# Kernel tuning notes

Hardware: AMD Instinct MI355X
Metric: run time of the kernel (lower is better)

Reference implementation:

```python
import jax, jax.numpy as jnp
import numpy as np

N = 8192
IN_F = 256
OUT_F = 128
ALPHA = 0.2  # LeakyReLU negative slope
NEG = -1e12


def setup_inputs() -> dict:
    key = jax.random.key(0)
    k1, k2, k3, k4, k5, k6 = jax.random.split(key, 6)
    inp = jax.random.normal(k1, (N, IN_F), dtype=jnp.float32)
    adj = jax.random.randint(k2, (N, N), 0, 2, dtype=jnp.int32)
    # xavier_uniform with gain=1.414
    def xavier(k, shape, gain=1.414):
        fan_in, fan_out = shape[0], shape[1]
        bound = gain * np.sqrt(6.0 / (fan_in + fan_out))
        return jax.random.uniform(k, shape, jnp.float32, -bound, bound)
    W = xavier(k3, (IN_F, OUT_F))
    a = xavier(k4, (2 * OUT_F, 1))
    W_2 = xavier(k5, (IN_F, OUT_F))
    a_2 = xavier(k6, (2 * OUT_F, 1))
    return {"inp": inp, "adj": adj, "W": W, "a": a, "W_2": W_2, "a_2": a_2}


def _gat_head(h, a_vec, mask):
    # Equivalent to e[i,j] = leakyrelu(a^T [h_i ; h_j]) without N^2*2F concat:
    # split a into source/destination halves.
    a_src = a_vec[:OUT_F, 0]   # [F]
    a_dst = a_vec[OUT_F:, 0]   # [F]
    e = (h @ a_src)[:, None] + (h @ a_dst)[None, :]        # [N, N]
    e = jnp.where(e > 0, e, ALPHA * e)                      # LeakyReLU
    e = jnp.where(mask, e, NEG)
    att = jax.nn.softmax(e, axis=1)                         # [N, N]
    # dropout omitted (eval mode, training=False)
    return att @ h                                          # [N, F]


def reference(inp, adj, W, a, W_2, a_2):
    h = inp @ W      # [N, F]
    h_2 = inp @ W_2  # [N, F]
    mask = adj > 0   # adj is nonneg ints so adj*adj>0 is the same mask
    h_prime = _gat_head(h, a, mask)
    h_prime_2 = _gat_head(h_2, a_2, mask)
    h_total = h_prime + 0.5 * h_prime_2
    return jax.nn.elu(h_total)  # concat=True
```

## Files before the change

### kernel.cpp

```cpp
#include <hip/hip_runtime.h>
#include <hip/hip_fp16.h>

#define NN 8192
#define INF 256
#define OUTF 128
#define LOG2E 1.44269504088896340736f

typedef float f32x4 __attribute__((ext_vector_type(4)));
typedef float f32x16 __attribute__((ext_vector_type(16)));
typedef __fp16 h16x8 __attribute__((ext_vector_type(8)));
typedef __fp16 h16x4 __attribute__((ext_vector_type(4)));
typedef __fp16 h16x2 __attribute__((ext_vector_type(2)));
typedef int i32x4 __attribute__((ext_vector_type(4)));

__device__ __forceinline__ void gload_lds16(const void* g, void* l) {
  __builtin_amdgcn_global_load_lds(
      (const __attribute__((address_space(1))) unsigned int*)g,
      (__attribute__((address_space(3))) unsigned int*)l, 16, 0, 0);
}

__device__ __forceinline__ unsigned encf(float f) {
  int b = __float_as_int(f);
  return b >= 0 ? ((unsigned)b | 0x80000000u) : ~(unsigned)b;
}
__device__ __forceinline__ float decf(unsigned u) {
  int b = (u & 0x80000000u) ? (int)(u & 0x7FFFFFFFu) : ~(int)u;
  return __int_as_float(b);
}

__global__ __launch_bounds__(256) void kb_pack(const int* __restrict__ adj,
                                               unsigned short* __restrict__ adjb) {
  int gid = blockIdx.x * 256 + threadIdx.x;
#pragma unroll
  for (int it = 0; it < 8; ++it) {
    size_t c = (size_t)it * 524288 + gid;
    const int* p = adj + c * 16;
    i32x4 v0 = *(const i32x4*)(p);
    i32x4 v1 = *(const i32x4*)(p + 4);
    i32x4 v2 = *(const i32x4*)(p + 8);
    i32x4 v3 = *(const i32x4*)(p + 12);
    unsigned int b = 0;
#pragma unroll
    for (int k = 0; k < 4; ++k) {
      b |= (v0[k] != 0 ? 1u : 0u) << k;
      b |= (v1[k] != 0 ? 1u : 0u) << (4 + k);
      b |= (v2[k] != 0 ? 1u : 0u) << (8 + k);
      b |= (v3[k] != 0 ? 1u : 0u) << (12 + k);
    }
    adjb[c] = (unsigned short)b;
  }
}

__global__ __launch_bounds__(256) void k0_wt(const float* __restrict__ W1,
                                             const float* __restrict__ W2,
                                             __fp16* __restrict__ WT,
                                             unsigned* __restrict__ GMu) {
  if (blockIdx.x == 0 && threadIdx.x < 2) GMu[threadIdx.x] = 0u;
  int m = blockIdx.x * 256 + threadIdx.x;
  int h = m >> 12;
  int r = m & 4095;
  int c = r >> 5;
  int kb = (r >> 1) & 15;
  int hh = r & 1;
  const float* W = h ? W2 : W1;
  float v[8];
#pragma unroll
  for (int s = 0; s < 8; ++s) {
    int koff = 4 * hh + (s & 3) + 8 * (s >> 2);
    v[s] = W[(kb * 16 + koff) * OUTF + c];
  }
  union { h16x2 h2[4]; i32x4 q; } u;
  u.h2[0] = __builtin_amdgcn_cvt_pkrtz(v[0], v[1]);
  u.h2[1] = __builtin_amdgcn_cvt_pkrtz(v[2], v[3]);
  u.h2[2] = __builtin_amdgcn_cvt_pkrtz(v[4], v[5]);
  u.h2[3] = __builtin_amdgcn_cvt_pkrtz(v[6], v[7]);
  *(i32x4*)(WT + (size_t)h * 32768 + c * 256 + kb * 16 + hh * 8) = u.q;
}

__global__ __launch_bounds__(128) void k1_h(
    const float* __restrict__ inp, const __fp16* __restrict__ WT,
    const float* __restrict__ a1, const float* __restrict__ a2,
    __fp16* __restrict__ hT2, float* __restrict__ S, float* __restrict__ D,
    unsigned* __restrict__ GMu) {
  __shared__ __align__(16) float hl[2][32][136];
  int tid = threadIdx.x;
  int w = tid >> 6;
  int l = tid & 63;
  int lr = l & 31, g = l >> 5;
  int i0 = blockIdx.x * 32;
  const __fp16* WTh = WT + (size_t)w * 32768;
  f32x16 acc[4];
#pragma unroll
  for (int nf = 0; nf < 4; ++nf)
#pragma unroll
    for (int e = 0; e < 16; ++e) acc[nf][e] = 0.0f;
  const float* ip = inp + (size_t)(i0 + lr) * INF;
#pragma unroll
  for (int kb = 0; kb < 16; ++kb) {
    f32x4 q0 = *(const f32x4*)(ip + kb * 16 + 4 * g);
    f32x4 q1 = *(const f32x4*)(ip + kb * 16 + 8 + 4 * g);
    union { h16x2 h2[4]; h16x8 h8; } ua;
    ua.h2[0] = __builtin_amdgcn_cvt_pkrtz(q0[0], q0[1]);
    ua.h2[1] = __builtin_amdgcn_cvt_pkrtz(q0[2], q0[3]);
    ua.h2[2] = __builtin_amdgcn_cvt_pkrtz(q1[0], q1[1]);
    ua.h2[3] = __builtin_amdgcn_cvt_pkrtz(q1[2], q1[3]);
#pragma unroll
    for (int nf = 0; nf < 4; ++nf) {
      h16x8 b = *(const h16x8*)(WTh + (nf * 32 + lr) * 256 + kb * 16 + g * 8);
      acc[nf] = __builtin_amdgcn_mfma_f32_32x32x16_f16(ua.h8, b, acc[nf], 0, 0, 0);
    }
  }
#pragma unroll
  for (int nf = 0; nf < 4; ++nf)
#pragma unroll
    for (int r = 0; r < 16; ++r) {
      int row = (r & 3) + 8 * (r >> 2) + 4 * g;
      hl[w][row][nf * 32 + lr] = acc[nf][r];
    }
  __syncthreads();
  const float* av = w ? a2 : a1;
  float s = 0.f, d = 0.f;
#pragma unroll
  for (int cc = 0; cc < 64; cc += 4) {
    int c = g * 64 + cc;
    f32x4 hv = *(const f32x4*)&hl[w][lr][c];
    f32x4 as = *(const f32x4*)(av + c);
    f32x4 ad = *(const f32x4*)(av + 128 + c);
    s += hv[0] * as[0] + hv[1] * as[1] + hv[2] * as[2] + hv[3] * as[3];
    d += hv[0] * ad[0] + hv[1] * ad[1] + hv[2] * ad[2] + hv[3] * ad[3];
  }
  s += __shfl_xor(s, 32);
  d += __shfl_xor(d, 32);
  float dl = d * LOG2E;
  if (g == 0) {
    S[(size_t)w * NN + i0 + lr] = s * LOG2E;
    D[(size_t)w * NN + i0 + lr] = dl;
  }
  float dmax = dl;
#pragma unroll
  for (int off = 1; off < 32; off <<= 1) dmax = fmaxf(dmax, __shfl_xor(dmax, off));
  if (l == 0) atomicMax(GMu + w, encf(dmax));
  __fp16* hTh = hT2 + (size_t)w * (NN * OUTF);
#pragma unroll
  for (int it = 0; it < 8; ++it) {
    int id = it * 64 + l;
    int jb = id >> 8;
    int sub = id & 255;
    int nf = sub >> 6, lq = sub & 63;
    int lqr = lq & 31, lqg = lq >> 5;
    float v[8];
#pragma unroll
    for (int s2 = 0; s2 < 8; ++s2) {
      int kloc = 4 * lqg + (s2 & 3) + 8 * (s2 >> 2);
      v[s2] = hl[w][jb * 16 + kloc][nf * 32 + lqr];
    }
    union { h16x2 h2[4]; i32x4 q; } u2;
    u2.h2[0] = __builtin_amdgcn_cvt_pkrtz(v[0], v[1]);
    u2.h2[1] = __builtin_amdgcn_cvt_pkrtz(v[2], v[3]);
    u2.h2[2] = __builtin_amdgcn_cvt_pkrtz(v[4], v[5]);
    u2.h2[3] = __builtin_amdgcn_cvt_pkrtz(v[6], v[7]);
    *(i32x4*)(hTh + (size_t)((i0 >> 4) + jb) * 2048 + sub * 8) = u2.q;
  }
}

__global__ __launch_bounds__(256, 2) void k2_attn(
    const unsigned short* __restrict__ adjb, const __fp16* __restrict__ hT2,
    const float* __restrict__ S, const float* __restrict__ D,
    const unsigned* __restrict__ GMu, __fp16* __restrict__ NUM,
    float* __restrict__ DEN) {
  __shared__ __align__(16) char smem[32768];
  int tid = threadIdx.x;
  int w = tid >> 6;
  int l = tid & 63;
  int lr = l & 31, g2 = l >> 5;
  int h = w >> 1, rq = w & 1;
  int rb = blockIdx.x >> 3, js = blockIdx.x & 7;
  int i0 = rb * 128;
  int jwin = js * 1024, jw16 = js * 64;
  int base = i0 + rq * 64;
  int row0 = base + lr, row1 = base + 32 + lr;
  float gm = decf(GMu[h]);
  float sf0 = S[(size_t)h * NN + row0];
  float sf1 = S[(size_t)h * NN + row1];
  float t0 = sf0 + gm, t1 = sf1 + gm;
  float cn0 = -fmaxf(t0, 0.2f * t0) - 1000.0f;
  float cn1 = -fmaxf(t1, 0.2f * t1) - 1000.0f;
  float Ac0 = sf0 + cn0, Bc0 = 0.2f * sf0 + cn0;
  float Ac1 = sf1 + cn1, Bc1 = 0.2f * sf1 + cn1;
  const float* Dh = D + (size_t)h * NN + jwin + 4 * g2;

  f32x16 acc[2][4];
#pragma unroll
  for (int f = 0; f < 2; ++f)
#pragma unroll
    for (int nf = 0; nf < 4; ++nf)
#pragma unroll
      for (int e = 0; e < 16; ++e) acc[f][nf][e] = 0.0f;
  float dsum0 = 0.f, dsum1 = 0.f;

  auto STAGE = [&](int jstep, int b) {
#pragma unroll
    for (int q = 0; q < 4; ++q) {
      int kk_l = q >> 1, hh = q & 1;
      const __fp16* gs = hT2 + (size_t)hh * (NN * OUTF) +
                         (size_t)(jw16 + jstep * 2 + kk_l) * 2048 + tid * 8;
      gload_lds16(gs, smem + b * 16384 + q * 4096 + tid * 16);
    }
  };

  const unsigned short* mrow0 = adjb + (size_t)row0 * 512 + jw16;
  const unsigned short* mrow1 = adjb + (size_t)row1 * 512 + jw16;
  i32x4 mreg0 = *(const i32x4*)(mrow0), mnext0 = *(const i32x4*)(mrow0 + 8);
  i32x4 mreg1 = *(const i32x4*)(mrow1), mnext1 = *(const i32x4*)(mrow1 + 8);

  const h16x2 ones = {(__fp16)1.0f, (__fp16)1.0f};
  h16x8 P[2][2], Pn[2][2];

  auto SOFTMAX = [&](int jn, unsigned dwm0, unsigned dwm1) {
#pragma unroll
    for (int kk = 0; kk < 2; ++kk) {
      int kkg = jn * 2 + kk;
      f32x4 d0 = *(const f32x4*)(Dh + kkg * 16);
      f32x4 d1 = *(const f32x4*)(Dh + kkg * 16 + 8);
      unsigned bts[2] = {kk ? (dwm0 >> 16) : (dwm0 & 0xffffu),
                         kk ? (dwm1 >> 16) : (dwm1 & 0xffffu)};
#pragma unroll
      for (int f = 0; f < 2; ++f) {
        float Af = f ? Ac1 : Ac0, Bf_ = f ? Bc1 : Bc0;
        unsigned bt = bts[f];
        float pv[8];
#pragma unroll
        for (int s = 0; s < 8; ++s) {
          float dd = (s < 4) ? d0[s] : d1[s - 4];
          int kloc = 4 * g2 + (s & 3) + 8 * (s >> 2);
          float uu = fmaxf(Af + dd, fmaf(0.2f, dd, Bf_));
          float bfv = (float)((bt >> kloc) & 1u);
          pv[s] = __builtin_amdgcn_exp2f(fmaf(bfv, 1000.0f, uu));
        }
        union { h16x2 h2[4]; h16x8 h8; } uq;
        uq.h2[0] = __builtin_amdgcn_cvt_pkrtz(pv[0], pv[1]);
        uq.h2[1] = __builtin_amdgcn_cvt_pkrtz(pv[2], pv[3]);
        uq.h2[2] = __builtin_amdgcn_cvt_pkrtz(pv[4], pv[5]);
        uq.h2[3] = __builtin_amdgcn_cvt_pkrtz(pv[6], pv[7]);
        float ds = f ? dsum1 : dsum0;
#if __has_builtin(__builtin_amdgcn_fdot2)
        ds = __builtin_amdgcn_fdot2(uq.h2[0], ones, ds, false);
        ds = __builtin_amdgcn_fdot2(uq.h2[1], ones, ds, false);
        ds = __builtin_amdgcn_fdot2(uq.h2[2], ones, ds, false);
        ds = __builtin_amdgcn_fdot2(uq.h2[3], ones, ds, false);
#else
        ds += ((pv[0] + pv[1]) + (pv[2] + pv[3])) + ((pv[4] + pv[5]) + (pv[6] + pv[7]));
#endif
        if (f) dsum1 = ds; else dsum0 = ds;
        Pn[f][kk] = uq.h8;
      }
    }
  };

  auto MFMA_STEP = [&](int b) {
#pragma unroll
    for (int kk = 0; kk < 2; ++kk) {
      const char* lb = smem + b * 16384 + (kk * 2 + h) * 4096 + l * 16;
#pragma unroll
      for (int nf = 0; nf < 4; ++nf) {
        h16x8 Bf = *(const h16x8*)(lb + nf * 1024);
        acc[0][nf] = __builtin_amdgcn_mfma_f32_32x32x16_f16(P[0][kk], Bf, acc[0][nf], 0, 0, 0);
        acc[1][nf] = __builtin_amdgcn_mfma_f32_32x32x16_f16(P[1][kk], Bf, acc[1][nf], 0, 0, 0);
      }
    }
  };

  STAGE(0, 0);
  SOFTMAX(0, (unsigned)mreg0[0], (unsigned)mreg1[0]);
#pragma unroll
  for (int f = 0; f < 2; ++f)
#pragma unroll
    for (int kk = 0; kk < 2; ++kk) P[f][kk] = Pn[f][kk];
  __syncthreads();

  for (int j4 = 0; j4 < 8; ++j4) {
#pragma unroll
    for (int u = 0; u < 4; ++u) {
      const int jstep = j4 * 4 + u;
      const int b = jstep & 1;
      if (jstep < 31) STAGE(jstep + 1, b ^ 1);
      if (u == 3) {
        mreg0 = mnext0; mreg1 = mnext1;
        if (j4 < 6) {
          mnext0 = *(const i32x4*)(mrow0 + (j4 + 2) * 8);
          mnext1 = *(const i32x4*)(mrow1 + (j4 + 2) * 8);
        }
      }
      if (jstep < 31) {
        const int un = (u + 1) & 3;
        SOFTMAX(jstep + 1, (unsigned)mreg0[un], (unsigned)mreg1[un]);
      }
      MFMA_STEP(b);
      if (jstep < 31) {
#pragma unroll
        for (int f = 0; f < 2; ++f)
#pragma unroll
          for (int kk = 0; kk < 2; ++kk) P[f][kk] = Pn[f][kk];
      }
      __syncthreads();
    }
  }

  dsum0 += __shfl_xor(dsum0, 32);
  dsum1 += __shfl_xor(dsum1, 32);
  if (g2 == 0) {
    DEN[(size_t)(js * 2 + h) * NN + row0] = dsum0;
    DEN[(size_t)(js * 2 + h) * NN + row1] = dsum1;
  }
#pragma unroll
  for (int f = 0; f < 2; ++f) {
    __fp16* nb = NUM + ((size_t)(js * 2 + h) * NN + base + f * 32) * 128 + lr;
#pragma unroll
    for (int nf = 0; nf < 4; ++nf)
#pragma unroll
      for (int r = 0; r < 16; ++r) {
        int crow = (r & 3) + 8 * (r >> 2) + 4 * g2;
        nb[(size_t)crow * 128 + nf * 32] = (__fp16)acc[f][nf][r];
      }
  }
}

__global__ __launch_bounds__(256) void k3_out(const __fp16* __restrict__ NUM,
                                              const float* __restrict__ DEN,
                                              float* __restrict__ out) {
  int gid = blockIdx.x * 256 + threadIdx.x;
  int i = gid >> 5;
  int c4 = (gid & 31) * 4;
  f32x4 n1 = {0.f, 0.f, 0.f, 0.f}, n2 = {0.f, 0.f, 0.f, 0.f};
  float d1 = 0.f, d2 = 0.f;
#pragma unroll
  for (int js = 0; js < 8; ++js) {
    h16x4 a1v = *(const h16x4*)(NUM + ((size_t)(js * 2 + 0) * NN + i) * 128 + c4);
    h16x4 a2v = *(const h16x4*)(NUM + ((size_t)(js * 2 + 1) * NN + i) * 128 + c4);
#pragma unroll
    for (int e = 0; e < 4; ++e) { n1[e] += (float)a1v[e]; n2[e] += (float)a2v[e]; }
    d1 += DEN[(size_t)(js * 2 + 0) * NN + i];
    d2 += DEN[(size_t)(js * 2 + 1) * NN + i];
  }
  float r1 = 1.0f / d1, r2 = 0.5f / d2;
  f32x4 o;
#pragma unroll
  for (int e = 0; e < 4; ++e) {
    float x = n1[e] * r1 + n2[e] * r2;
    o[e] = x > 0.f ? x : (exp2f(x * LOG2E) - 1.0f);
  }
  *(f32x4*)(out + (size_t)i * 128 + c4) = o;
}

extern "C" void kernel_launch(void* const* d_in, const int* in_sizes, int n_in,
                              void* d_out, int out_size, void* d_ws, size_t ws_size,
                              hipStream_t stream) {
  const float* inp = (const float*)d_in[0];
  const int* adj = (const int*)d_in[1];
  const float* W1 = (const float*)d_in[2];
  const float* a1 = (const float*)d_in[3];
  const float* W2 = (const float*)d_in[4];
  const float* a2 = (const float*)d_in[5];
  float* out = (float*)d_out;
  char* ws = (char*)d_ws;
  __fp16* WT = (__fp16*)(ws);
  __fp16* hT2 = (__fp16*)(ws + 131072);
  float* S = (float*)(ws + 4325376);
  float* D = (float*)(ws + 4390912);
  unsigned* GMu = (unsigned*)(ws + 4456448);
  unsigned short* adjb = (unsigned short*)(ws + 4456704);
  __fp16* NUM = (__fp16*)(ws + 12845312);
  float* DEN = (float*)(ws + 46399744);

  kb_pack<<<dim3(2048), dim3(256), 0, stream>>>(adj, adjb);
  k0_wt<<<dim3(32), dim3(256), 0, stream>>>(W1, W2, WT, GMu);
  k1_h<<<dim3(256), dim3(128), 0, stream>>>(inp, WT, a1, a2, hT2, S, D, GMu);
  k2_attn<<<dim3(512), dim3(256), 0, stream>>>(adjb, hT2, S, D, GMu, NUM, DEN);
  k3_out<<<dim3(1024), dim3(256), 0, stream>>>(NUM, DEN, out);
}
```

Before: 136.8 us.

## Fuse adjacency packing into projection kernel and load attention B operands to registers

The adjacency bit-packing kernel is merged into the projection kernel as extra blocks, so both run in one launch and can overlap. The projection work is split across four waves instead of two. In the attention kernel, the LDS double-buffer staging of hT2 is replaced by direct global loads into register double buffers, and the D vector is staged once into LDS. This removes the per-step __syncthreads and LDS traffic. In exchange it raises register pressure and relies on L2 to serve the repeated hT2 loads.

```diff
diff --git a/kernel.cpp b/kernel.cpp
--- a/kernel.cpp
+++ b/kernel.cpp
@@ -26,29 +26,6 @@
 __device__ __forceinline__ float decf(unsigned u) {
   int b = (u & 0x80000000u) ? (int)(u & 0x7FFFFFFFu) : ~(int)u;
   return __int_as_float(b);
-}
-
-__global__ __launch_bounds__(256) void kb_pack(const int* __restrict__ adj,
-                                               unsigned short* __restrict__ adjb) {
-  int gid = blockIdx.x * 256 + threadIdx.x;
-#pragma unroll
-  for (int it = 0; it < 8; ++it) {
-    size_t c = (size_t)it * 524288 + gid;
-    const int* p = adj + c * 16;
-    i32x4 v0 = *(const i32x4*)(p);
-    i32x4 v1 = *(const i32x4*)(p + 4);
-    i32x4 v2 = *(const i32x4*)(p + 8);
-    i32x4 v3 = *(const i32x4*)(p + 12);
-    unsigned int b = 0;
-#pragma unroll
-    for (int k = 0; k < 4; ++k) {
-      b |= (v0[k] != 0 ? 1u : 0u) << k;
-      b |= (v1[k] != 0 ? 1u : 0u) << (4 + k);
-      b |= (v2[k] != 0 ? 1u : 0u) << (8 + k);
-      b |= (v3[k] != 0 ? 1u : 0u) << (12 + k);
-    }
-    adjb[c] = (unsigned short)b;
-  }
 }
 
 __global__ __launch_bounds__(256) void k0_wt(const float* __restrict__ W1,
@@ -77,23 +54,47 @@
   *(i32x4*)(WT + (size_t)h * 32768 + c * 256 + kb * 16 + hh * 8) = u.q;
 }
 
-__global__ __launch_bounds__(128) void k1_h(
+__global__ __launch_bounds__(256) void kf(
+    const int* __restrict__ adj, unsigned short* __restrict__ adjb,
     const float* __restrict__ inp, const __fp16* __restrict__ WT,
     const float* __restrict__ a1, const float* __restrict__ a2,
     __fp16* __restrict__ hT2, float* __restrict__ S, float* __restrict__ D,
     unsigned* __restrict__ GMu) {
   __shared__ __align__(16) float hl[2][32][136];
+  if (blockIdx.x >= 256) {
+    int gid = (blockIdx.x - 256) * 256 + threadIdx.x;
+#pragma unroll
+    for (int it = 0; it < 8; ++it) {
+      size_t c = (size_t)it * 524288 + gid;
+      const int* p = adj + c * 16;
+      i32x4 v0 = *(const i32x4*)(p);
+      i32x4 v1 = *(const i32x4*)(p + 4);
+      i32x4 v2 = *(const i32x4*)(p + 8);
+      i32x4 v3 = *(const i32x4*)(p + 12);
+      unsigned int b = 0;
+#pragma unroll
+      for (int k = 0; k < 4; ++k) {
+        b |= (v0[k] != 0 ? 1u : 0u) << k;
+        b |= (v1[k] != 0 ? 1u : 0u) << (4 + k);
+        b |= (v2[k] != 0 ? 1u : 0u) << (8 + k);
+        b |= (v3[k] != 0 ? 1u : 0u) << (12 + k);
+      }
+      adjb[c] = (unsigned short)b;
+    }
+    return;
+  }
   int tid = threadIdx.x;
   int w = tid >> 6;
+  int head = w >> 1, half = w & 1;
   int l = tid & 63;
   int lr = l & 31, g = l >> 5;
   int i0 = blockIdx.x * 32;
-  const __fp16* WTh = WT + (size_t)w * 32768;
-  f32x16 acc[4];
-#pragma unroll
-  for (int nf = 0; nf < 4; ++nf)
-#pragma unroll
-    for (int e = 0; e < 16; ++e) acc[nf][e] = 0.0f;
+  const __fp16* WTh = WT + (size_t)head * 32768;
+  f32x16 acc[2];
+#pragma unroll
+  for (int nf2 = 0; nf2 < 2; ++nf2)
+#pragma unroll
+    for (int e = 0; e < 16; ++e) acc[nf2][e] = 0.0f;
   const float* ip = inp + (size_t)(i0 + lr) * INF;
 #pragma unroll
   for (int kb = 0; kb < 16; ++kb) {
@@ -105,45 +106,50 @@
     ua.h2[2] = __builtin_amdgcn_cvt_pkrtz(q1[0], q1[1]);
     ua.h2[3] = __builtin_amdgcn_cvt_pkrtz(q1[2], q1[3]);
 #pragma unroll
-    for (int nf = 0; nf < 4; ++nf) {
+    for (int nf2 = 0; nf2 < 2; ++nf2) {
+      int nf = half * 2 + nf2;
       h16x8 b = *(const h16x8*)(WTh + (nf * 32 + lr) * 256 + kb * 16 + g * 8);
-      acc[nf] = __builtin_amdgcn_mfma_f32_32x32x16_f16(ua.h8, b, acc[nf], 0, 0, 0);
-    }
-  }
-#pragma unroll
-  for (int nf = 0; nf < 4; ++nf)
+      acc[nf2] = __builtin_amdgcn_mfma_f32_32x32x16_f16(ua.h8, b, acc[nf2], 0, 0, 0);
+    }
+  }
+#pragma unroll
+  for (int nf2 = 0; nf2 < 2; ++nf2) {
+    int nf = half * 2 + nf2;
 #pragma unroll
     for (int r = 0; r < 16; ++r) {
       int row = (r & 3) + 8 * (r >> 2) + 4 * g;
-      hl[w][row][nf * 32 + lr] = acc[nf][r];
-    }
+      hl[head][row][nf * 32 + lr] = acc[nf2][r];
+    }
+  }
   __syncthreads();
-  const float* av = w ? a2 : a1;
-  float s = 0.f, d = 0.f;
-#pragma unroll
-  for (int cc = 0; cc < 64; cc += 4) {
-    int c = g * 64 + cc;
-    f32x4 hv = *(const f32x4*)&hl[w][lr][c];
-    f32x4 as = *(const f32x4*)(av + c);
-    f32x4 ad = *(const f32x4*)(av + 128 + c);
-    s += hv[0] * as[0] + hv[1] * as[1] + hv[2] * as[2] + hv[3] * as[3];
-    d += hv[0] * ad[0] + hv[1] * ad[1] + hv[2] * ad[2] + hv[3] * ad[3];
-  }
-  s += __shfl_xor(s, 32);
-  d += __shfl_xor(d, 32);
-  float dl = d * LOG2E;
-  if (g == 0) {
-    S[(size_t)w * NN + i0 + lr] = s * LOG2E;
-    D[(size_t)w * NN + i0 + lr] = dl;
-  }
-  float dmax = dl;
-#pragma unroll
-  for (int off = 1; off < 32; off <<= 1) dmax = fmaxf(dmax, __shfl_xor(dmax, off));
-  if (l == 0) atomicMax(GMu + w, encf(dmax));
-  __fp16* hTh = hT2 + (size_t)w * (NN * OUTF);
-#pragma unroll
-  for (int it = 0; it < 8; ++it) {
-    int id = it * 64 + l;
+  if (half == 0) {
+    const float* av = head ? a2 : a1;
+    float s = 0.f, d = 0.f;
+#pragma unroll
+    for (int cc = 0; cc < 64; cc += 4) {
+      int c = g * 64 + cc;
+      f32x4 hv = *(const f32x4*)&hl[head][lr][c];
+      f32x4 as = *(const f32x4*)(av + c);
+      f32x4 ad = *(const f32x4*)(av + 128 + c);
+      s += hv[0] * as[0] + hv[1] * as[1] + hv[2] * as[2] + hv[3] * as[3];
+      d += hv[0] * ad[0] + hv[1] * ad[1] + hv[2] * ad[2] + hv[3] * ad[3];
+    }
+    s += __shfl_xor(s, 32);
+    d += __shfl_xor(d, 32);
+    float dl = d * LOG2E;
+    if (g == 0) {
+      S[(size_t)head * NN + i0 + lr] = s * LOG2E;
+      D[(size_t)head * NN + i0 + lr] = dl;
+    }
+    float dmax = dl;
+#pragma unroll
+    for (int off = 1; off < 32; off <<= 1) dmax = fmaxf(dmax, __shfl_xor(dmax, off));
+    if (l == 0) atomicMax(GMu + head, encf(dmax));
+  }
+  __fp16* hTh = hT2 + (size_t)head * (NN * OUTF);
+#pragma unroll
+  for (int it2 = 0; it2 < 4; ++it2) {
+    int id = (half * 4 + it2) * 64 + l;
     int jb = id >> 8;
     int sub = id & 255;
     int nf = sub >> 6, lq = sub & 63;
@@ -152,7 +158,7 @@
 #pragma unroll
     for (int s2 = 0; s2 < 8; ++s2) {
       int kloc = 4 * lqg + (s2 & 3) + 8 * (s2 >> 2);
-      v[s2] = hl[w][jb * 16 + kloc][nf * 32 + lqr];
+      v[s2] = hl[head][jb * 16 + kloc][nf * 32 + lqr];
     }
     union { h16x2 h2[4]; i32x4 q; } u2;
     u2.h2[0] = __builtin_amdgcn_cvt_pkrtz(v[0], v[1]);
@@ -168,7 +174,7 @@
     const float* __restrict__ S, const float* __restrict__ D,
     const unsigned* __restrict__ GMu, __fp16* __restrict__ NUM,
     float* __restrict__ DEN) {
-  __shared__ __align__(16) char smem[32768];
+  __shared__ __align__(16) float Dw[2][1024];
   int tid = threadIdx.x;
   int w = tid >> 6;
   int l = tid & 63;
@@ -187,7 +193,13 @@
   float cn1 = -fmaxf(t1, 0.2f * t1) - 1000.0f;
   float Ac0 = sf0 + cn0, Bc0 = 0.2f * sf0 + cn0;
   float Ac1 = sf1 + cn1, Bc1 = 0.2f * sf1 + cn1;
-  const float* Dh = D + (size_t)h * NN + jwin + 4 * g2;
+
+#pragma unroll
+  for (int q = 0; q < 2; ++q) {
+    int idx = q * 256 + tid;
+    int hh = idx >> 8, jj = idx & 255;
+    gload_lds16(D + (size_t)hh * NN + jwin + jj * 4, (char*)&Dw[0][0] + idx * 16);
+  }
 
   f32x16 acc[2][4];
 #pragma unroll
@@ -198,13 +210,13 @@
       for (int e = 0; e < 16; ++e) acc[f][nf][e] = 0.0f;
   float dsum0 = 0.f, dsum1 = 0.f;
 
-  auto STAGE = [&](int jstep, int b) {
-#pragma unroll
-    for (int q = 0; q < 4; ++q) {
-      int kk_l = q >> 1, hh = q & 1;
-      const __fp16* gs = hT2 + (size_t)hh * (NN * OUTF) +
-                         (size_t)(jw16 + jstep * 2 + kk_l) * 2048 + tid * 8;
-      gload_lds16(gs, smem + b * 16384 + q * 4096 + tid * 16);
+  const __fp16* Bbase = hT2 + (size_t)h * (NN * OUTF) + (size_t)jw16 * 2048 + l * 8;
+  h16x8 BA[8], BB[8];
+  auto LOADB = [&](int jstep, h16x8* Bn) {
+#pragma unroll
+    for (int q = 0; q < 8; ++q) {
+      int kk = q >> 2, nf = q & 3;
+      Bn[q] = *(const h16x8*)(Bbase + (size_t)(jstep * 2 + kk) * 2048 + nf * 512);
     }
   };
 
@@ -214,14 +226,15 @@
   i32x4 mreg1 = *(const i32x4*)(mrow1), mnext1 = *(const i32x4*)(mrow1 + 8);
 
   const h16x2 ones = {(__fp16)1.0f, (__fp16)1.0f};
-  h16x8 P[2][2], Pn[2][2];
+  h16x8 P[2][2];
+  const float* DwH = &Dw[h][0] + 4 * g2;
 
   auto SOFTMAX = [&](int jn, unsigned dwm0, unsigned dwm1) {
 #pragma unroll
     for (int kk = 0; kk < 2; ++kk) {
       int kkg = jn * 2 + kk;
-      f32x4 d0 = *(const f32x4*)(Dh + kkg * 16);
-      f32x4 d1 = *(const f32x4*)(Dh + kkg * 16 + 8);
+      f32x4 d0 = *(const f32x4*)(DwH + kkg * 16);
+      f32x4 d1 = *(const f32x4*)(DwH + kkg * 16 + 8);
       unsigned bts[2] = {kk ? (dwm0 >> 16) : (dwm0 & 0xffffu),
                          kk ? (dwm1 >> 16) : (dwm1 & 0xffffu)};
 #pragma unroll
@@ -252,57 +265,40 @@
         ds += ((pv[0] + pv[1]) + (pv[2] + pv[3])) + ((pv[4] + pv[5]) + (pv[6] + pv[7]));
 #endif
         if (f) dsum1 = ds; else dsum0 = ds;
-        Pn[f][kk] = uq.h8;
+        P[f][kk] = uq.h8;
       }
     }
   };
 
-  auto MFMA_STEP = [&](int b) {
-#pragma unroll
-    for (int kk = 0; kk < 2; ++kk) {
-      const char* lb = smem + b * 16384 + (kk * 2 + h) * 4096 + l * 16;
+  auto MFMA_STEP = [&](const h16x8* Bc) {
+#pragma unroll
+    for (int kk = 0; kk < 2; ++kk)
 #pragma unroll
       for (int nf = 0; nf < 4; ++nf) {
-        h16x8 Bf = *(const h16x8*)(lb + nf * 1024);
-        acc[0][nf] = __builtin_amdgcn_mfma_f32_32x32x16_f16(P[0][kk], Bf, acc[0][nf], 0, 0, 0);
-        acc[1][nf] = __builtin_amdgcn_mfma_f32_32x32x16_f16(P[1][kk], Bf, acc[1][nf], 0, 0, 0);
-      }
-    }
+        acc[0][nf] = __builtin_amdgcn_mfma_f32_32x32x16_f16(P[0][kk], Bc[kk * 4 + nf], acc[0][nf], 0, 0, 0);
+        acc[1][nf] = __builtin_amdgcn_mfma_f32_32x32x16_f16(P[1][kk], Bc[kk * 4 + nf], acc[1][nf], 0, 0, 0);
+      }
   };
 
-  STAGE(0, 0);
-  SOFTMAX(0, (unsigned)mreg0[0], (unsigned)mreg1[0]);
-#pragma unroll
-  for (int f = 0; f < 2; ++f)
-#pragma unroll
-    for (int kk = 0; kk < 2; ++kk) P[f][kk] = Pn[f][kk];
+  LOADB(0, BA);
   __syncthreads();
 
   for (int j4 = 0; j4 < 8; ++j4) {
 #pragma unroll
     for (int u = 0; u < 4; ++u) {
       const int jstep = j4 * 4 + u;
-      const int b = jstep & 1;
-      if (jstep < 31) STAGE(jstep + 1, b ^ 1);
-      if (u == 3) {
+      h16x8* Bc = (u & 1) ? BB : BA;
+      h16x8* Bn = (u & 1) ? BA : BB;
+      if (jstep < 31) LOADB(jstep + 1, Bn);
+      SOFTMAX(jstep, (unsigned)mreg0[u], (unsigned)mreg1[u]);
+      if (u == 3 && j4 < 7) {
         mreg0 = mnext0; mreg1 = mnext1;
         if (j4 < 6) {
           mnext0 = *(const i32x4*)(mrow0 + (j4 + 2) * 8);
           mnext1 = *(const i32x4*)(mrow1 + (j4 + 2) * 8);
         }
       }
-      if (jstep < 31) {
-        const int un = (u + 1) & 3;
-        SOFTMAX(jstep + 1, (unsigned)mreg0[un], (unsigned)mreg1[un]);
-      }
-      MFMA_STEP(b);
-      if (jstep < 31) {
-#pragma unroll
-        for (int f = 0; f < 2; ++f)
-#pragma unroll
-          for (int kk = 0; kk < 2; ++kk) P[f][kk] = Pn[f][kk];
-      }
-      __syncthreads();
+      MFMA_STEP(Bc);
     }
   }
 
@@ -372,9 +368,8 @@
   __fp16* NUM = (__fp16*)(ws + 12845312);
   float* DEN = (float*)(ws + 46399744);
 
-  kb_pack<<<dim3(2048), dim3(256), 0, stream>>>(adj, adjb);
   k0_wt<<<dim3(32), dim3(256), 0, stream>>>(W1, W2, WT, GMu);
-  k1_h<<<dim3(256), dim3(128), 0, stream>>>(inp, WT, a1, a2, hT2, S, D, GMu);
+  kf<<<dim3(2304), dim3(256), 0, stream>>>(adj, adjb, inp, WT, a1, a2, hT2, S, D, GMu);
   k2_attn<<<dim3(512), dim3(256), 0, stream>>>(adjb, hT2, S, D, GMu, NUM, DEN);
   k3_out<<<dim3(1024), dim3(256), 0, stream>>>(NUM, DEN, out);
 }
```

After: 175.7 us. +28.5%, slower.

## Fuse adjacency bit-packing into attention kernel via wave ballots into LDS

Applied to the files above, without the earlier changes.

Removes the separate kb_pack kernel and its packed-mask buffer round trip. The attention kernel now reads the int32 adjacency directly, builds bitmasks with wave ballots, and stores them in a double-buffered LDS area one 256-column group ahead. The softmax then reads each row's mask from LDS with a new bit ordering. This drops one launch and the packed write/read, but puts the full 256MB adjacency read inside the attention kernel's main loop, adds LDS usage that may affect occupancy, and removes the register-level prefetch of the next softmax step.

```diff
diff --git a/kernel.cpp b/kernel.cpp
--- a/kernel.cpp
+++ b/kernel.cpp
@@ -26,29 +26,6 @@
 __device__ __forceinline__ float decf(unsigned u) {
   int b = (u & 0x80000000u) ? (int)(u & 0x7FFFFFFFu) : ~(int)u;
   return __int_as_float(b);
-}
-
-__global__ __launch_bounds__(256) void kb_pack(const int* __restrict__ adj,
-                                               unsigned short* __restrict__ adjb) {
-  int gid = blockIdx.x * 256 + threadIdx.x;
-#pragma unroll
-  for (int it = 0; it < 8; ++it) {
-    size_t c = (size_t)it * 524288 + gid;
-    const int* p = adj + c * 16;
-    i32x4 v0 = *(const i32x4*)(p);
-    i32x4 v1 = *(const i32x4*)(p + 4);
-    i32x4 v2 = *(const i32x4*)(p + 8);
-    i32x4 v3 = *(const i32x4*)(p + 12);
-    unsigned int b = 0;
-#pragma unroll
-    for (int k = 0; k < 4; ++k) {
-      b |= (v0[k] != 0 ? 1u : 0u) << k;
-      b |= (v1[k] != 0 ? 1u : 0u) << (4 + k);
-      b |= (v2[k] != 0 ? 1u : 0u) << (8 + k);
-      b |= (v3[k] != 0 ? 1u : 0u) << (12 + k);
-    }
-    adjb[c] = (unsigned short)b;
-  }
 }
 
 __global__ __launch_bounds__(256) void k0_wt(const float* __restrict__ W1,
@@ -164,11 +141,12 @@
 }
 
 __global__ __launch_bounds__(256, 2) void k2_attn(
-    const unsigned short* __restrict__ adjb, const __fp16* __restrict__ hT2,
+    const int* __restrict__ adj, const __fp16* __restrict__ hT2,
     const float* __restrict__ S, const float* __restrict__ D,
     const unsigned* __restrict__ GMu, __fp16* __restrict__ NUM,
     float* __restrict__ DEN) {
   __shared__ __align__(16) char smem[32768];
+  __shared__ __align__(16) char maskL[10240];
   int tid = threadIdx.x;
   int w = tid >> 6;
   int l = tid & 63;
@@ -176,7 +154,7 @@
   int h = w >> 1, rq = w & 1;
   int rb = blockIdx.x >> 3, js = blockIdx.x & 7;
   int i0 = rb * 128;
-  int jwin = js * 1024, jw16 = js * 64;
+  int jwin = js * 1024;
   int base = i0 + rq * 64;
   int row0 = base + lr, row1 = base + 32 + lr;
   float gm = decf(GMu[h]);
@@ -203,38 +181,61 @@
     for (int q = 0; q < 4; ++q) {
       int kk_l = q >> 1, hh = q & 1;
       const __fp16* gs = hT2 + (size_t)hh * (NN * OUTF) +
-                         (size_t)(jw16 + jstep * 2 + kk_l) * 2048 + tid * 8;
+                         (size_t)(js * 64 + jstep * 2 + kk_l) * 2048 + tid * 8;
       gload_lds16(gs, smem + b * 16384 + q * 4096 + tid * 16);
     }
   };
 
-  const unsigned short* mrow0 = adjb + (size_t)row0 * 512 + jw16;
-  const unsigned short* mrow1 = adjb + (size_t)row1 * 512 + jw16;
-  i32x4 mreg0 = *(const i32x4*)(mrow0), mnext0 = *(const i32x4*)(mrow0 + 8);
-  i32x4 mreg1 = *(const i32x4*)(mrow1), mnext1 = *(const i32x4*)(mrow1 + 8);
+  auto PRODUCE = [&](int gg, int r4) {
+    const int* ab = adj + (size_t)(i0 + r4) * NN + jwin + gg * 256 + l * 4;
+    i32x4 vv0 = *(const i32x4*)(ab);
+    i32x4 vv1 = *(const i32x4*)(ab + NN);
+    i32x4 vv2 = *(const i32x4*)(ab + 2 * NN);
+    i32x4 vv3 = *(const i32x4*)(ab + 3 * NN);
+    char* mrow = maskL + (gg & 1) * 5120 + r4 * 40 + l * 8;
+#pragma unroll
+    for (int rr = 0; rr < 4; ++rr) {
+      i32x4 vv = rr == 0 ? vv0 : rr == 1 ? vv1 : rr == 2 ? vv2 : vv3;
+      unsigned long long b0 = __ballot(vv[0] != 0);
+      unsigned long long b1 = __ballot(vv[1] != 0);
+      unsigned long long b2 = __ballot(vv[2] != 0);
+      unsigned long long b3 = __ballot(vv[3] != 0);
+      unsigned long long bsel = b0;
+      bsel = (l == 1) ? b1 : bsel;
+      bsel = (l == 2) ? b2 : bsel;
+      bsel = (l == 3) ? b3 : bsel;
+      if (l < 4) *(unsigned long long*)(mrow + rr * 40) = bsel;
+    }
+  };
+
+  auto MASK32 = [&](int slot, int r, int u) -> unsigned {
+    const unsigned char* mb = (const unsigned char*)(maskL + slot * 5120 + r * 40 + u);
+    unsigned m0 = mb[0], m1 = mb[8], m2 = mb[16], m3 = mb[24];
+    return m0 | (m1 << 8) | (m2 << 16) | (m3 << 24);
+  };
 
   const h16x2 ones = {(__fp16)1.0f, (__fp16)1.0f};
-  h16x8 P[2][2], Pn[2][2];
-
-  auto SOFTMAX = [&](int jn, unsigned dwm0, unsigned dwm1) {
+  h16x8 P[2][2];
+
+  auto SOFTMAX = [&](int jstep, int slot, int u) {
+    unsigned bts0 = MASK32(slot, rq * 64 + lr, u) >> g2;
+    unsigned bts1 = MASK32(slot, rq * 64 + 32 + lr, u) >> g2;
 #pragma unroll
     for (int kk = 0; kk < 2; ++kk) {
-      int kkg = jn * 2 + kk;
+      int kkg = jstep * 2 + kk;
       f32x4 d0 = *(const f32x4*)(Dh + kkg * 16);
       f32x4 d1 = *(const f32x4*)(Dh + kkg * 16 + 8);
-      unsigned bts[2] = {kk ? (dwm0 >> 16) : (dwm0 & 0xffffu),
-                         kk ? (dwm1 >> 16) : (dwm1 & 0xffffu)};
 #pragma unroll
       for (int f = 0; f < 2; ++f) {
         float Af = f ? Ac1 : Ac0, Bf_ = f ? Bc1 : Bc0;
-        unsigned bt = bts[f];
+        unsigned bts = f ? bts1 : bts0;
         float pv[8];
 #pragma unroll
         for (int s = 0; s < 8; ++s) {
           float dd = (s < 4) ? d0[s] : d1[s - 4];
-          int kloc = 4 * g2 + (s & 3) + 8 * (s >> 2);
+          const int bitp = 8 * (s & 3) + 4 * kk + 2 * (s >> 2);
           float uu = fmaxf(Af + dd, fmaf(0.2f, dd, Bf_));
-          float bfv = (float)((bt >> kloc) & 1u);
+          float bfv = (float)((bts >> bitp) & 1u);
           pv[s] = __builtin_amdgcn_exp2f(fmaf(bfv, 1000.0f, uu));
         }
         union { h16x2 h2[4]; h16x8 h8; } uq;
@@ -252,7 +253,7 @@
         ds += ((pv[0] + pv[1]) + (pv[2] + pv[3])) + ((pv[4] + pv[5]) + (pv[6] + pv[7]));
 #endif
         if (f) dsum1 = ds; else dsum0 = ds;
-        Pn[f][kk] = uq.h8;
+        P[f][kk] = uq.h8;
       }
     }
   };
@@ -271,37 +272,19 @@
   };
 
   STAGE(0, 0);
-  SOFTMAX(0, (unsigned)mreg0[0], (unsigned)mreg1[0]);
-#pragma unroll
-  for (int f = 0; f < 2; ++f)
-#pragma unroll
-    for (int kk = 0; kk < 2; ++kk) P[f][kk] = Pn[f][kk];
+#pragma unroll
+  for (int c = 0; c < 8; ++c) PRODUCE(0, w * 32 + c * 4);
   __syncthreads();
 
-  for (int j4 = 0; j4 < 8; ++j4) {
-#pragma unroll
-    for (int u = 0; u < 4; ++u) {
-      const int jstep = j4 * 4 + u;
+  for (int g = 0; g < 4; ++g) {
+#pragma unroll
+    for (int u = 0; u < 8; ++u) {
+      const int jstep = g * 8 + u;
       const int b = jstep & 1;
       if (jstep < 31) STAGE(jstep + 1, b ^ 1);
-      if (u == 3) {
-        mreg0 = mnext0; mreg1 = mnext1;
-        if (j4 < 6) {
-          mnext0 = *(const i32x4*)(mrow0 + (j4 + 2) * 8);
-          mnext1 = *(const i32x4*)(mrow1 + (j4 + 2) * 8);
-        }
-      }
-      if (jstep < 31) {
-        const int un = (u + 1) & 3;
-        SOFTMAX(jstep + 1, (unsigned)mreg0[un], (unsigned)mreg1[un]);
-      }
+      if (g < 3) PRODUCE(g + 1, w * 32 + u * 4);
+      SOFTMAX(jstep, g & 1, u);
       MFMA_STEP(b);
-      if (jstep < 31) {
-#pragma unroll
-        for (int f = 0; f < 2; ++f)
-#pragma unroll
-          for (int kk = 0; kk < 2; ++kk) P[f][kk] = Pn[f][kk];
-      }
       __syncthreads();
     }
   }
@@ -368,13 +351,11 @@
   float* S = (float*)(ws + 4325376);
   float* D = (float*)(ws + 4390912);
   unsigned* GMu = (unsigned*)(ws + 4456448);
-  unsigned short* adjb = (unsigned short*)(ws + 4456704);
   __fp16* NUM = (__fp16*)(ws + 12845312);
   float* DEN = (float*)(ws + 46399744);
 
-  kb_pack<<<dim3(2048), dim3(256), 0, stream>>>(adj, adjb);
   k0_wt<<<dim3(32), dim3(256), 0, stream>>>(W1, W2, WT, GMu);
   k1_h<<<dim3(256), dim3(128), 0, stream>>>(inp, WT, a1, a2, hT2, S, D, GMu);
-  k2_attn<<<dim3(512), dim3(256), 0, stream>>>(adjb, hT2, S, D, GMu, NUM, DEN);
+  k2_attn<<<dim3(512), dim3(256), 0, stream>>>(adj, hT2, S, D, GMu, NUM, DEN);
   k3_out<<<dim3(1024), dim3(256), 0, stream>>>(NUM, DEN, out);
 }
```

New measurement: 157.7 us. +15.3%, slower.
